# Optimization experiments

Measured on AMD Instinct MI355X. Metric: run time of the kernel, lower is better.

## Reference

```python
import jax, jax.numpy as jnp
import numpy as np

N, M, E = 14541, 237, 120000
XS, GS, HID, OUT, H = 100, 100, 100, 100, 2
NEG_SLOPE = 0.2


def _l2(v, axis):
    # F.normalize(p=2): x / clamp_min(||x||, 1e-12)
    return v / jnp.maximum(jnp.linalg.norm(v, axis=axis, keepdims=True), 1e-12)


def _rel_att(h_ijk, ends, n, W, b, w_att, out):
    # edge MLP -> [E, H, out]
    c = (h_ijk @ W.T + b).reshape(-1, H, out)
    # attention logits per edge/head, b_ijk = -leaky_relu(a_ijk)
    a = jnp.sum(w_att * c, axis=2, keepdims=True)            # [E, H, 1]
    e = jnp.exp(-jax.nn.leaky_relu(a, NEG_SLOPE))            # [E, H, 1]
    denom = jax.ops.segment_sum(e, ends, num_segments=n)     # [n, H, 1]
    alpha = e / denom[ends]                                  # scatter-softmax
    # self zero-edges in original == segment_sum zero-init; elu(0)=0 matches
    h = jax.ops.segment_sum(alpha * c, ends, num_segments=n) # [n, H, out]
    return jax.nn.elu(h)


def setup_inputs() -> dict:
    key = jax.random.key(0)
    ks = jax.random.split(key, 24)
    f32 = jnp.float32
    def w(k, shp, s=0.1):
        return jax.random.normal(k, shp, dtype=f32) * s
    inp = {
        "x": jax.random.normal(ks[0], (N, XS), dtype=f32),
        "g": jax.random.normal(ks[1], (M, GS), dtype=f32),
        # layer-1 inbound/outbound attention (fc1: [H*HID, 2*XS+GS])
        "W1in": w(ks[2], (H * HID, 2 * XS + GS)), "b1in": jnp.zeros((H * HID,), f32), "a1in": w(ks[3], (1, H, HID)),
        "W1out": w(ks[4], (H * HID, 2 * XS + GS)), "b1out": jnp.zeros((H * HID,), f32), "a1out": w(ks[5], (1, H, HID)),
        "Wa1": w(ks[6], (1, 2 * HID)), "ba1": jnp.zeros((1,), f32),
        # layer-2 attention (fc1: [H*OUT, 2*H*HID+GS])
        "W2in": w(ks[7], (H * OUT, 2 * H * HID + GS)), "b2in": jnp.zeros((H * OUT,), f32), "a2in": w(ks[8], (1, H, OUT)),
        "W2out": w(ks[9], (H * OUT, 2 * H * HID + GS)), "b2out": jnp.zeros((H * OUT,), f32), "a2out": w(ks[10], (1, H, OUT)),
        "Wa2": w(ks[11], (1, 2 * OUT)), "ba2": jnp.zeros((1,), f32),
        # entity residual projection and relation projection
        "Went": w(ks[12], (H * OUT, XS)), "bent": jnp.zeros((H * OUT,), f32),
        "Wrel": w(ks[13], (H * OUT, GS)), "brel": jnp.zeros((H * OUT,), f32),
        "edge_idx": jax.random.randint(ks[14], (2, E), 0, N),
        "edge_type": jax.random.randint(ks[15], (E,), 0, M),
    }
    return inp


def reference(x, g, W1in, b1in, a1in, W1out, b1out, a1out, Wa1, ba1,
              W2in, b2in, a2in, W2out, b2out, a2out, Wa2, ba2,
              Went, bent, Wrel, brel, edge_idx, edge_type):
    n = x.shape[0]
    xn = _l2(x, 1)
    row, col = edge_idx[0], edge_idx[1]
    # layer 1
    h_ijk = jnp.concatenate([xn[row], xn[col], g[edge_type]], axis=1)  # [E, 2*XS+GS]
    hin = _rel_att(h_ijk, col, n, W1in, b1in, a1in, HID)
    hout = _rel_att(h_ijk, row, n, W1out, b1out, a1out, HID)
    al = jax.nn.sigmoid(jnp.concatenate([hin, hout], axis=2) @ Wa1.T + ba1)  # [n, H, 1]
    h = al * hin + (1.0 - al) * hout
    h = _l2(jax.nn.elu(h), 2).reshape(n, H * HID)  # head-concat
    # layer 2
    h_ijk = jnp.concatenate([h[row], h[col], g[edge_type]], axis=1)  # [E, 2*H*HID+GS]
    hin = _rel_att(h_ijk, col, n, W2in, b2in, a2in, OUT)
    hout = _rel_att(h_ijk, row, n, W2out, b2out, a2out, OUT)
    al = jax.nn.sigmoid(jnp.concatenate([hin, hout], axis=2) @ Wa2.T + ba2)
    h = al * hin + (1.0 - al) * hout
    h = _l2(jax.nn.elu(h), 2)                       # [n, H, OUT]
    # entity residual + relation projection
    h_prime = (xn @ Went.T + bent).reshape(n, H, OUT) + h
    h_prime = _l2(h_prime, 2).reshape(n, H * OUT)
    g_prime = g @ Wrel.T + brel                     # [M, H*OUT]
    return h_prime, g_prime
```

## Files before the change

### kernel.cpp

```cpp
#include <hip/hip_runtime.h>
#include <math.h>

#define NSLOPE 0.2f

typedef unsigned short ushort_t;
typedef unsigned char uchar_t;
typedef __attribute__((ext_vector_type(8))) short bf16x8;
typedef __attribute__((ext_vector_type(8))) unsigned short ushort8;
typedef __attribute__((ext_vector_type(4))) float f32x4;

__device__ __forceinline__ float elu1(float x) { return x > 0.f ? x : expm1f(x); }

__device__ __forceinline__ ushort_t f2bf(float f) {
  union { float f; unsigned int u; } v; v.f = f;
  unsigned int r = v.u + 0x7fffu + ((v.u >> 16) & 1u);
  return (ushort_t)(r >> 16);
}
__device__ __forceinline__ float bf2f(ushort_t u) {
  union { unsigned int i; float f; } v; v.i = ((unsigned int)u) << 16; return v.f;
}
__device__ __forceinline__ uchar_t f2fp8(float f) {
  int pk = __builtin_amdgcn_cvt_pk_fp8_f32(f, f, 0, false);
  return (uchar_t)(pk & 0xff);
}


__device__ void dev_build_w(int idx,
                            const float* __restrict__ W1in, const float* __restrict__ W1out,
                            const float* __restrict__ W2in, const float* __restrict__ W2out,
                            const float* __restrict__ Went,
                            ushort_t* __restrict__ wcat1, ushort_t* __restrict__ wcat2,
                            ushort_t* __restrict__ wentb) {
  const int S1 = 832 * 128, S2 = 832 * 256, S3 = 256 * 128;
  if (idx < S1) {
    int ro = idx >> 7, k = idx & 127;
    float val = 0.f;
    if (ro < 800 && k < 100) {
      int o = ro / 200, cc = ro - o * 200;
      const float* W = (o < 2) ? W1in : W1out;
      val = W[(size_t)cc * 300 + (o & 1) * 100 + k];
    }
    wcat1[idx] = f2bf(val);
  } else if (idx < S1 + S2) {
    int i2 = idx - S1;
    int ro = i2 >> 8, k = i2 & 255;
    float val = 0.f;
    if (ro < 800 && k < 200) {
      int o = ro / 200, cc = ro - o * 200;
      const float* W = (o < 2) ? W2in : W2out;
      val = W[(size_t)cc * 500 + (o & 1) * 200 + k];
    }
    wcat2[i2] = f2bf(val);
  } else if (idx < S1 + S2 + S3) {
    int i3 = idx - S1 - S2;
    int ro = i3 >> 7, k = i3 & 127;
    float val = (ro < 200 && k < 100) ? Went[ro * 100 + k] : 0.f;
    wentb[i3] = f2bf(val);
  }
}

__device__ void dev_makeu(int idx,
                          const float* __restrict__ W1in, const float* __restrict__ a1in,
                          const float* __restrict__ W1out, const float* __restrict__ a1out,
                          const float* __restrict__ W2in, const float* __restrict__ a2in,
                          const float* __restrict__ W2out, const float* __restrict__ a2out,
                          float* __restrict__ u1in, float* __restrict__ u1out,
                          float* __restrict__ u2in, float* __restrict__ u2out) {
  if (idx >= 3200) return;
  const float* W; const float* avec; float* u; int Kp, local;
  if (idx < 600)       { W = W1in;  avec = a1in;  u = u1in;  Kp = 300; local = idx; }
  else if (idx < 1200) { W = W1out; avec = a1out; u = u1out; Kp = 300; local = idx - 600; }
  else if (idx < 2200) { W = W2in;  avec = a2in;  u = u2in;  Kp = 500; local = idx - 1200; }
  else                 { W = W2out; avec = a2out; u = u2out; Kp = 500; local = idx - 2200; }
  int h = local / Kp, kp = local - h * Kp;
  const float* Wb = W + (size_t)(h * 100) * Kp + kp;
  const float* ab = avec + h * 100;
  float s = 0.f;
  for (int k = 0; k < 100; ++k) s += ab[k] * Wb[(size_t)k * Kp];
  u[local] = s;
}

__device__ void dev_l2norm_q(int bb, int tid, const float* __restrict__ x,
                             ushort_t* __restrict__ xnb,
                             const float* __restrict__ u1in, const float* __restrict__ u1out,
                             float* __restrict__ qA, float* __restrict__ qB,
                             float* __restrict__ qC, float* __restrict__ qD, int N) {
  int wid = bb * 4 + (tid >> 6);
  int lane = tid & 63;
  if (wid >= N) return;
  const float* p = x + (size_t)wid * 100;
  float v0 = p[lane];
  bool t2 = lane < 36;
  float v1 = t2 ? p[lane + 64] : 0.f;
  float ss = v0 * v0 + v1 * v1;
#pragma unroll
  for (int m = 1; m < 64; m <<= 1) ss += __shfl_xor(ss, m, 64);
  float inv = 1.f / fmaxf(sqrtf(ss), 1e-12f);
  float a0 = v0 * inv, a1 = v1 * inv;
  ushort_t* ob = xnb + (size_t)wid * 128;
  ob[lane] = f2bf(a0);
  ob[64 + lane] = t2 ? f2bf(a1) : (ushort_t)0;
  int k0 = lane, k1 = 64 + lane;
  float s[8];
  s[0] = a0 * u1in[k0]        + (t2 ? a1 * u1in[k1]        : 0.f);
  s[1] = a0 * u1in[300 + k0]  + (t2 ? a1 * u1in[300 + k1]  : 0.f);
  s[2] = a0 * u1in[100 + k0]  + (t2 ? a1 * u1in[100 + k1]  : 0.f);
  s[3] = a0 * u1in[400 + k0]  + (t2 ? a1 * u1in[400 + k1]  : 0.f);
  s[4] = a0 * u1out[k0]       + (t2 ? a1 * u1out[k1]       : 0.f);
  s[5] = a0 * u1out[300 + k0] + (t2 ? a1 * u1out[300 + k1] : 0.f);
  s[6] = a0 * u1out[100 + k0] + (t2 ? a1 * u1out[100 + k1] : 0.f);
  s[7] = a0 * u1out[400 + k0] + (t2 ? a1 * u1out[400 + k1] : 0.f);
#pragma unroll
  for (int m = 1; m < 64; m <<= 1) {
#pragma unroll
    for (int i = 0; i < 8; ++i) s[i] += __shfl_xor(s[i], m, 64);
  }
  if (lane == 0) {
    qA[wid * 2] = s[0]; qA[wid * 2 + 1] = s[1];
    qB[wid * 2] = s[2]; qB[wid * 2 + 1] = s[3];
    qC[wid * 2] = s[4]; qC[wid * 2 + 1] = s[5];
    qD[wid * 2] = s[6]; qD[wid * 2 + 1] = s[7];
  }
}

__device__ void dev_qrel2(int bb, int tid, const float* __restrict__ g,
                          const float* __restrict__ u1in, const float* __restrict__ u1out,
                          const float* __restrict__ u2in, const float* __restrict__ u2out,
                          float* __restrict__ q3i1, float* __restrict__ q3o1,
                          float* __restrict__ q3i2, float* __restrict__ q3o2, int Mn) {
  int wid = bb * 4 + (tid >> 6);
  int lane = tid & 63;
  if (wid >= 2 * Mn) return;
  int lay = wid >= Mn;
  int m = wid - lay * Mn;
  const float* uin  = lay ? u2in  : u1in;
  const float* uout = lay ? u2out : u1out;
  int Kp = lay ? 500 : 300;
  int off3 = lay ? 400 : 200;
  float* q3i = lay ? q3i2 : q3i1;
  float* q3o = lay ? q3o2 : q3o1;
  const float* a = g + (size_t)m * 100;
  float s[4] = {0.f, 0.f, 0.f, 0.f};
  for (int k = lane; k < 100; k += 64) {
    float av = a[k];
    s[0] += av * uin[off3 + k];
    s[1] += av * uin[Kp + off3 + k];
    s[2] += av * uout[off3 + k];
    s[3] += av * uout[Kp + off3 + k];
  }
#pragma unroll
  for (int mm = 1; mm < 64; mm <<= 1) {
#pragma unroll
    for (int i = 0; i < 4; ++i) s[i] += __shfl_xor(s[i], mm, 64);
  }
  if (lane == 0) {
    q3i[m * 2] = s[0]; q3i[m * 2 + 1] = s[1];
    q3o[m * 2] = s[2]; q3o[m * 2 + 1] = s[3];
  }
}

__device__ void dev_count(int bb, int tid, const int* __restrict__ row,
                          const int* __restrict__ col,
                          int* __restrict__ cntIn, int* __restrict__ cntOut, int E) {
  int e = bb * 256 + tid;
  if (e >= E) return;
  atomicAdd(&cntIn[col[e]], 1);
  atomicAdd(&cntOut[row[e]], 1);
}

__device__ void dev_edge_e(int bb, int tid,
                           const int* __restrict__ row, const int* __restrict__ col,
                           const int* __restrict__ ety,
                           const float* __restrict__ qA, const float* __restrict__ qB,
                           const float* __restrict__ q3i,
                           const float* __restrict__ qC, const float* __restrict__ qD,
                           const float* __restrict__ q3o,
                           const int* __restrict__ invIn, const int* __restrict__ invOut,
                           float4* __restrict__ recI, float4* __restrict__ recO, int E) {
  int e = bb * 256 + tid;
  if (e >= E) return;
  int r = row[e], c = col[e], t = ety[e];
  float2 vA = *(const float2*)(qA + (size_t)r * 2);
  float2 vB = *(const float2*)(qB + (size_t)c * 2);
  float2 v3 = *(const float2*)(q3i + (size_t)t * 2);
  float2 vC = *(const float2*)(qC + (size_t)r * 2);
  float2 vD = *(const float2*)(qD + (size_t)c * 2);
  float2 v4 = *(const float2*)(q3o + (size_t)t * 2);
  float a0 = vA.x + vB.x + v3.x, a1 = vA.y + vB.y + v3.y;
  float b0 = vC.x + vD.x + v4.x, b1 = vC.y + vD.y + v4.y;
  float2 rI, rO;
  rI.x = expf(-(a0 > 0.f ? a0 : NSLOPE * a0));
  rI.y = expf(-(a1 > 0.f ? a1 : NSLOPE * a1));
  rO.x = expf(-(b0 > 0.f ? b0 : NSLOPE * b0));
  rO.y = expf(-(b1 > 0.f ? b1 : NSLOPE * b1));
  *(float2*)(recI + invIn[e]) = rI;
  *(float2*)(recO + invOut[e]) = rO;
}

__device__ void dev_mfma(int bx, int by, int tid,
                         ushort_t* __restrict__ smA, ushort_t* __restrict__ smB,
                         const ushort_t* __restrict__ Ab, int lda,
                         const ushort_t* __restrict__ Bb, int Kpad,
                         int R, int NC, int OUTW, const float* __restrict__ bias,
                         float* __restrict__ C0,
                         ushort_t* __restrict__ Bd0, ushort_t* __restrict__ Bd1,
                         ushort_t* __restrict__ Bd2, ushort_t* __restrict__ Bd3,
                         uchar_t* __restrict__ Q0, uchar_t* __restrict__ Q3) {
  const int lane = tid & 63;
  const int w = tid >> 6;
  const int wm = w >> 1, wn = w & 1;
  const int m0 = by * 64;
  const int n0 = bx * 64;
  const int srow = tid >> 2;
  const int sq = tid & 3;
  const int sw3 = srow & 7;
  const int sbase = srow * 64;
  const int so0 = sbase + ((((sq << 1) + 0) ^ sw3) << 3);
  const int so1 = sbase + ((((sq << 1) + 1) ^ sw3) << 3);
  const bool aok = (m0 + srow) < R;
  const ushort_t* Ag = Ab + (size_t)(m0 + srow) * lda + sq * 16;
  const ushort_t* Bg = Bb + (size_t)(n0 + srow) * Kpad + sq * 16;
  const int lswz = lane & 7;
  const int hi = lane >> 4;
  const int rA0 = (wm * 32 + (lane & 15)) * 64;
  const int rB0 = (wn * 32 + (lane & 15)) * 64;
  f32x4 acc[2][2] = {};
  for (int k0 = 0; k0 < Kpad; k0 += 64) {
    ushort8 a0 = {0, 0, 0, 0, 0, 0, 0, 0}, a1 = {0, 0, 0, 0, 0, 0, 0, 0};
    if (aok) {
      a0 = *(const ushort8*)(Ag + k0);
      a1 = *(const ushort8*)(Ag + k0 + 8);
    }
    ushort8 b0 = *(const ushort8*)(Bg + k0);
    ushort8 b1 = *(const ushort8*)(Bg + k0 + 8);
    __syncthreads();
    *(ushort8*)(smA + so0) = a0;
    *(ushort8*)(smA + so1) = a1;
    *(ushort8*)(smB + so0) = b0;
    *(ushort8*)(smB + so1) = b1;
    __syncthreads();
#pragma unroll
    for (int ks = 0; ks < 2; ++ks) {
      int co = (((ks << 2) + hi) ^ lswz) << 3;
      bf16x8 aA = *(const bf16x8*)(smA + rA0 + co);
      bf16x8 aB = *(const bf16x8*)(smA + rA0 + 1024 + co);
      bf16x8 bA = *(const bf16x8*)(smB + rB0 + co);
      bf16x8 bB = *(const bf16x8*)(smB + rB0 + 1024 + co);
      acc[0][0] = __builtin_amdgcn_mfma_f32_16x16x32_bf16(aA, bA, acc[0][0], 0, 0, 0);
      acc[0][1] = __builtin_amdgcn_mfma_f32_16x16x32_bf16(aA, bB, acc[0][1], 0, 0, 0);
      acc[1][0] = __builtin_amdgcn_mfma_f32_16x16x32_bf16(aB, bA, acc[1][0], 0, 0, 0);
      acc[1][1] = __builtin_amdgcn_mfma_f32_16x16x32_bf16(aB, bB, acc[1][1], 0, 0, 0);
    }
  }
  ushort_t* Bds[4] = {Bd0, Bd1, Bd2, Bd3};
#pragma unroll
  for (int mt = 0; mt < 2; ++mt) {
    int rr0 = m0 + wm * 32 + mt * 16 + (lane >> 4) * 4;
#pragma unroll
    for (int nt = 0; nt < 2; ++nt) {
      int cc = n0 + wn * 32 + nt * 16 + (lane & 15);
      if (cc < NC) {
        int o = cc / OUTW;
        int c2 = cc - o * OUTW;
        float bv = bias ? bias[c2] : 0.f;
        uchar_t* Q = (o == 0) ? Q0 : ((o == 3) ? Q3 : nullptr);
        ushort_t* Bd = Bds[o];
        if (Q) {
#pragma unroll
          for (int reg = 0; reg < 4; ++reg) {
            int r = rr0 + reg;
            if (r < R) Q[(size_t)r * OUTW + c2] = f2fp8(acc[mt][nt][reg] + bv);
          }
        } else if (Bd) {
#pragma unroll
          for (int reg = 0; reg < 4; ++reg) {
            int r = rr0 + reg;
            if (r < R) Bd[(size_t)r * OUTW + c2] = f2bf(acc[mt][nt][reg] + bv);
          }
        } else {
#pragma unroll
          for (int reg = 0; reg < 4; ++reg) {
            int r = rr0 + reg;
            if (r < R) C0[(size_t)r * OUTW + c2] = acc[mt][nt][reg] + bv;
          }
        }
      }
    }
  }
}

template <int NOUT, int BF>
__device__ void dev_gemm_multi(int bx, int by, int tid, float4 (*As)[25],
                               const float* __restrict__ A, int lda,
                               const float* __restrict__ W0, const float* __restrict__ W1,
                               int ldw,
                               const float* __restrict__ b0, const float* __restrict__ b1,
                               void* __restrict__ C0v, void* __restrict__ C1v, int R) {
  const int K4 = 25;
  int row0 = by * 32;
  {
    int r = tid >> 3;
    int rr = row0 + r;
    const float4* Ar = (const float4*)(A + (size_t)rr * lda);
    for (int k4 = (tid & 7); k4 < K4; k4 += 8)
      As[r][k4] = (rr < R) ? Ar[k4] : make_float4(0.f, 0.f, 0.f, 0.f);
  }
  __syncthreads();
  int c = bx * 64 + (tid & 63);
  if (c < 200) {
    int rb = (tid >> 6) << 3;
    const float4* Wr[NOUT];
    Wr[0] = (const float4*)(W0 + (size_t)c * ldw);
    if (NOUT > 1) Wr[1] = (const float4*)(W1 + (size_t)c * ldw);
    float acc[NOUT][8];
#pragma unroll
    for (int o = 0; o < NOUT; ++o)
#pragma unroll
      for (int i = 0; i < 8; ++i) acc[o][i] = 0.f;
#pragma unroll 2
    for (int k4 = 0; k4 < K4; ++k4) {
      float4 a[8];
#pragma unroll
      for (int i = 0; i < 8; ++i) a[i] = As[rb + i][k4];
#pragma unroll
      for (int o = 0; o < NOUT; ++o) {
        float4 wv = Wr[o][k4];
#pragma unroll
        for (int i = 0; i < 8; ++i)
          acc[o][i] += a[i].x * wv.x + a[i].y * wv.y + a[i].z * wv.z + a[i].w * wv.w;
      }
    }
    float bv[NOUT];
    bv[0] = b0 ? b0[c] : 0.f;
    if (NOUT > 1) bv[1] = b1 ? b1[c] : 0.f;
    void* Cp[NOUT];
    Cp[0] = C0v;
    if (NOUT > 1) Cp[1] = C1v;
#pragma unroll
    for (int i = 0; i < 8; ++i) {
      int rr = row0 + rb + i;
      if (rr < R) {
#pragma unroll
        for (int o = 0; o < NOUT; ++o) {
          float val = acc[o][i] + bv[o];
          if (BF) ((ushort_t*)Cp[o])[(size_t)rr * 200 + c] = f2bf(val);
          else    ((float*)Cp[o])[(size_t)rr * 200 + c] = val;
        }
      }
    }
  }
}


__global__ __launch_bounds__(256) void MEGA0(
    const float* W1in, const float* W1out, const float* W2in, const float* W2out,
    const float* Went,
    ushort_t* wcat1, ushort_t* wcat2, ushort_t* wentb,
    const float* a1in, const float* a1out, const float* a2in, const float* a2out,
    float* u1in, float* u1out, float* u2in, float* u2out,
    int* cntIn, int* cntOut, int N, int nb_bw, int nb_mk) {
  int b = blockIdx.x, tid = threadIdx.x;
  if (b < nb_bw) {
    dev_build_w(b * 256 + tid, W1in, W1out, W2in, W2out, Went, wcat1, wcat2, wentb);
  } else if (b < nb_bw + nb_mk) {
    dev_makeu((b - nb_bw) * 256 + tid, W1in, a1in, W1out, a1out, W2in, a2in, W2out, a2out,
              u1in, u1out, u2in, u2out);
  } else {
    int idx = (b - nb_bw - nb_mk) * 256 + tid;
    if (idx < N) cntIn[idx] = 0;
    else if (idx < 2 * N) cntOut[idx - N] = 0;
  }
}

__global__ __launch_bounds__(256) void MEGA1(
    const float* x, ushort_t* xnb, const float* u1in, const float* u1out,
    float* qA, float* qB, float* qC, float* qD, int N,
    const float* g, const float* u2in, const float* u2out,
    float* q3i1, float* q3o1, float* q3i2, float* q3o2, int Mn,
    const int* row, const int* col, int* cntIn, int* cntOut, int E,
    int nb_l2, int nb_qr) {
  int b = blockIdx.x, tid = threadIdx.x;
  if (b < nb_l2) {
    dev_l2norm_q(b, tid, x, xnb, u1in, u1out, qA, qB, qC, qD, N);
  } else if (b < nb_l2 + nb_qr) {
    dev_qrel2(b - nb_l2, tid, g, u1in, u1out, u2in, u2out, q3i1, q3o1, q3i2, q3o2, Mn);
  } else {
    dev_count(b - nb_l2 - nb_qr, tid, row, col, cntIn, cntOut, E);
  }
}

__global__ __launch_bounds__(256) void k_scanA(const int* __restrict__ cntIn,
                                               const int* __restrict__ cntOut,
                                               int* __restrict__ part, int N, int nbc) {
  __shared__ int wsum[4];
  int b = blockIdx.x;
  const int* cnt = (b < nbc) ? cntIn : cntOut;
  int cb = (b < nbc) ? b : b - nbc;
  int idx = cb * 256 + threadIdx.x;
  int v = (idx < N) ? cnt[idx] : 0;
#pragma unroll
  for (int m = 1; m < 64; m <<= 1) v += __shfl_xor(v, m, 64);
  if ((threadIdx.x & 63) == 0) wsum[threadIdx.x >> 6] = v;
  __syncthreads();
  if (threadIdx.x == 0) part[b] = wsum[0] + wsum[1] + wsum[2] + wsum[3];
}

__global__ __launch_bounds__(256) void k_scanB(int* __restrict__ part,
                                               int* __restrict__ rsIn, int* __restrict__ rsOut,
                                               int nbc, int N) {
  __shared__ int buf[512];
  int t = threadIdx.x;
  buf[t]       = (t < nbc) ? part[t] : 0;
  buf[256 + t] = (t < nbc) ? part[nbc + t] : 0;
  __syncthreads();
  for (int off = 1; off < 256; off <<= 1) {
    int v0 = (t >= off) ? buf[t - off] : 0;
    int v1 = (t >= off) ? buf[256 + t - off] : 0;
    __syncthreads();
    buf[t] += v0; buf[256 + t] += v1;
    __syncthreads();
  }
  if (t < nbc) {
    part[t]       = (t == 0) ? 0 : buf[t - 1];
    part[nbc + t] = (t == 0) ? 0 : buf[256 + t - 1];
  }
  if (t == 0) { rsIn[N] = buf[nbc - 1]; rsOut[N] = buf[256 + nbc - 1]; }
}

__global__ __launch_bounds__(256) void k_scanC(const int* __restrict__ cntIn,
                                               const int* __restrict__ cntOut,
                                               const int* __restrict__ part,
                                               int* __restrict__ rsIn, int* __restrict__ rsOut,
                                               int* __restrict__ posIn, int* __restrict__ posOut,
                                               int N, int nbc) {
  __shared__ int buf[256];
  int b = blockIdx.x;
  const int* cnt = (b < nbc) ? cntIn : cntOut;
  int* rs  = (b < nbc) ? rsIn : rsOut;
  int* pos = (b < nbc) ? posIn : posOut;
  int cb = (b < nbc) ? b : b - nbc;
  int base = part[b];
  int t = threadIdx.x;
  int idx = cb * 256 + t;
  buf[t] = (idx < N) ? cnt[idx] : 0;
  __syncthreads();
  for (int off = 1; off < 256; off <<= 1) {
    int v = (t >= off) ? buf[t - off] : 0;
    __syncthreads();
    buf[t] += v;
    __syncthreads();
  }
  if (idx < N) {
    int excl = base + ((t == 0) ? 0 : buf[t - 1]);
    rs[idx] = excl; pos[idx] = excl;
  }
}

__global__ void k_fill(const int* __restrict__ row, const int* __restrict__ col,
                       const int* __restrict__ ety,
                       int* __restrict__ posIn, int* __restrict__ posOut,
                       float4* __restrict__ recI, float4* __restrict__ recO,
                       int* __restrict__ invIn, int* __restrict__ invOut, int E) {
  int e = blockIdx.x * blockDim.x + threadIdx.x;
  if (e >= E) return;
  int r = row[e], c = col[e], tt = ety[e];
  int p = atomicAdd(&posIn[c], 1);
  ((int2*)(recI + p))[1] = make_int2(r, tt);
  invIn[e] = p;
  int q = atomicAdd(&posOut[r], 1);
  ((int2*)(recO + q))[1] = make_int2(c, tt);
  invOut[e] = q;
}

__global__ __launch_bounds__(256) void MEGA2(
    const ushort_t* xnb, const ushort_t* wcat1,
    uchar_t* PA8, ushort_t* PBb, ushort_t* PCb, uchar_t* PD8, int N,
    const int* row, const int* col, const int* ety,
    const float* qA, const float* qB, const float* q3i1,
    const float* qC, const float* qD, const float* q3o1,
    const int* invIn, const int* invOut, float4* recI, float4* recO, int E,
    const float* g, const float* W1in200, const float* W1out200,
    const float* b1in, const float* b1out, ushort_t* P3ib, ushort_t* P3ob,
    const float* W2in400, const float* W2out400,
    const float* b2in, const float* b2out, ushort_t* P3ib2, ushort_t* P3ob2, int Mn,
    const ushort_t* wentb, const float* bent, ushort_t* hentb,
    const float* Wrel, const float* brel, float* outg,
    int nb_mf, int nb_ee, int nb_gm, int nb_we) {
  __shared__ float4 shbuf4[1024];
  ushort_t* smA = (ushort_t*)shbuf4;
  ushort_t* smB = smA + 64 * 64;
  float4 (*As)[25] = (float4(*)[25])shbuf4;
  int b = blockIdx.x, tid = threadIdx.x;
  if (b < nb_mf) {
    dev_mfma(b % 13, b / 13, tid, smA, smB, xnb, 128, wcat1, 128, N, 800, 200, nullptr,
             nullptr, nullptr, PBb, PCb, nullptr, PA8, PD8);
  } else if ((b -= nb_mf) < nb_ee) {
    dev_edge_e(b, tid, row, col, ety, qA, qB, q3i1, qC, qD, q3o1,
               invIn, invOut, recI, recO, E);
  } else if ((b -= nb_ee) < nb_gm) {
    dev_gemm_multi<2, 1>(b & 3, b >> 2, tid, As, g, 100, W1in200, W1out200, 300,
                         b1in, b1out, P3ib, P3ob, Mn);
  } else if ((b -= nb_gm) < nb_gm) {
    dev_gemm_multi<2, 1>(b & 3, b >> 2, tid, As, g, 100, W2in400, W2out400, 500,
                         b2in, b2out, P3ib2, P3ob2, Mn);
  } else if ((b -= nb_gm) < nb_we) {
    dev_mfma(b & 3, b >> 2, tid, smA, smB, xnb, 128, wentb, 128, N, 200, 200, bent,
             nullptr, hentb, nullptr, nullptr, nullptr, nullptr, nullptr);
  } else {
    b -= nb_we;
    dev_gemm_multi<1, 0>(b & 3, b >> 2, tid, As, g, 100, Wrel, nullptr, 100,
                         brel, nullptr, outg, nullptr, Mn);
  }
}

__global__ __launch_bounds__(256) void MEGA3(
    const ushort_t* h1b, const ushort_t* wcat2,
    uchar_t* PA8, ushort_t* PBb, ushort_t* PCb, uchar_t* PD8, int N,
    const int* row, const int* col, const int* ety,
    const float* qA, const float* qB, const float* q3i2,
    const float* qC, const float* qD, const float* q3o2,
    const int* invIn, const int* invOut, float4* recI, float4* recO, int E,
    int nb_mf) {
  __shared__ float4 shbuf4[1024];
  ushort_t* smA = (ushort_t*)shbuf4;
  ushort_t* smB = smA + 64 * 64;
  int b = blockIdx.x, tid = threadIdx.x;
  if (b < nb_mf) {
    dev_mfma(b % 13, b / 13, tid, smA, smB, h1b, 256, wcat2, 256, N, 800, 200, nullptr,
             nullptr, nullptr, PBb, PCb, nullptr, PA8, PD8);
  } else {
    dev_edge_e(b - nb_mf, tid, row, col, ety, qA, qB, q3i2, qC, qD, q3o2,
               invIn, invOut, recI, recO, E);
  }
}

__global__ void k_node_att(const float4* __restrict__ recI, const int* __restrict__ rsIn,
                           const float4* __restrict__ recO, const int* __restrict__ rsOut,
                           const uchar_t* __restrict__ PA8, const ushort_t* __restrict__ PBb,
                           const ushort_t* __restrict__ PCb, const uchar_t* __restrict__ PD8,
                           const ushort_t* __restrict__ P3ib, const ushort_t* __restrict__ P3ob,
                           const float* __restrict__ Wg, const float* __restrict__ bg,
                           const float* __restrict__ u2in, const float* __restrict__ u2out,
                           float* __restrict__ qA, float* __restrict__ qB,
                           float* __restrict__ qC, float* __restrict__ qD,
                           ushort_t* __restrict__ Hb,
                           const ushort_t* __restrict__ hentb, float* __restrict__ outp, int N) {
  __shared__ float4 sRecI[4][64];
  __shared__ float4 sRecO[4][64];
  int wv = threadIdx.x >> 6;
  int wid  = (int)((blockIdx.x * (unsigned)blockDim.x + threadIdx.x) >> 6);
  int lane = threadIdx.x & 63;
  if (wid >= N) return;
  int n = wid;
  int half = lane >> 5, i = lane & 31;
  bool act = i < 25;
  int j = half * 100 + i * 4;
  int sIn = rsIn[n], degIn = rsIn[n + 1] - sIn;
  int sOut = rsOut[n], degOut = rsOut[n + 1] - sOut;
  float4 accIn = {0.f, 0.f, 0.f, 0.f}, accOut = {0.f, 0.f, 0.f, 0.f};
  float dI0 = 0.f, dI1 = 0.f, dO0 = 0.f, dO1 = 0.f;
  int mx = max(degIn, degOut);
  for (int b = 0; b < mx; b += 64) {
    int l = b + lane;
    if (l < degIn) {
      float4 rc = recI[sIn + l];
      dI0 += rc.x; dI1 += rc.y;
      sRecI[wv][lane] = rc;
    }
    if (l < degOut) {
      float4 rc = recO[sOut + l];
      dO0 += rc.x; dO1 += rc.y;
      sRecO[wv][lane] = rc;
    }
    int mI = degIn - b;  if (mI > 64) mI = 64;
    int mO = degOut - b; if (mO > 64) mO = 64;
    int m2 = max(mI, mO);
    for (int jj = 0; jj < m2; ++jj) {
      if (act && jj < mI) {
        float4 rc = sRecI[wv][jj];
        int rI = __float_as_int(rc.z), tI = __float_as_int(rc.w);
        float wgt = half ? rc.y : rc.x;
        int paw = *(const int*)(PA8 + (size_t)rI * 200 + j);
        ushort4 p3 = *(const ushort4*)(P3ib + (size_t)tI * 200 + j);
        accIn.x += wgt * (__builtin_amdgcn_cvt_f32_fp8(paw, 0) + bf2f(p3.x));
        accIn.y += wgt * (__builtin_amdgcn_cvt_f32_fp8(paw, 1) + bf2f(p3.y));
        accIn.z += wgt * (__builtin_amdgcn_cvt_f32_fp8(paw, 2) + bf2f(p3.z));
        accIn.w += wgt * (__builtin_amdgcn_cvt_f32_fp8(paw, 3) + bf2f(p3.w));
      }
      if (act && jj < mO) {
        float4 rc = sRecO[wv][jj];
        int rO = __float_as_int(rc.z), tO = __float_as_int(rc.w);
        float wgt = half ? rc.y : rc.x;
        int pdw = *(const int*)(PD8 + (size_t)rO * 200 + j);
        ushort4 p3 = *(const ushort4*)(P3ob + (size_t)tO * 200 + j);
        accOut.x += wgt * (__builtin_amdgcn_cvt_f32_fp8(pdw, 0) + bf2f(p3.x));
        accOut.y += wgt * (__builtin_amdgcn_cvt_f32_fp8(pdw, 1) + bf2f(p3.y));
        accOut.z += wgt * (__builtin_amdgcn_cvt_f32_fp8(pdw, 2) + bf2f(p3.z));
        accOut.w += wgt * (__builtin_amdgcn_cvt_f32_fp8(pdw, 3) + bf2f(p3.w));
      }
    }
  }
#pragma unroll
  for (int m = 1; m < 64; m <<= 1) {
    dI0 += __shfl_xor(dI0, m, 64); dI1 += __shfl_xor(dI1, m, 64);
    dO0 += __shfl_xor(dO0, m, 64); dO1 += __shfl_xor(dO1, m, 64);
  }
  float4 hin = {0.f, 0.f, 0.f, 0.f}, hout = {0.f, 0.f, 0.f, 0.f};
  if (degIn > 0 && act) {
    float invd = 1.f / (half ? dI1 : dI0);
    ushort4 ps = *(const ushort4*)(PBb + (size_t)n * 200 + j);
    hin.x = elu1(bf2f(ps.x) + accIn.x * invd);
    hin.y = elu1(bf2f(ps.y) + accIn.y * invd);
    hin.z = elu1(bf2f(ps.z) + accIn.z * invd);
    hin.w = elu1(bf2f(ps.w) + accIn.w * invd);
  }
  if (degOut > 0 && act) {
    float invd = 1.f / (half ? dO1 : dO0);
    ushort4 ps = *(const ushort4*)(PCb + (size_t)n * 200 + j);
    hout.x = elu1(bf2f(ps.x) + accOut.x * invd);
    hout.y = elu1(bf2f(ps.y) + accOut.y * invd);
    hout.z = elu1(bf2f(ps.z) + accOut.z * invd);
    hout.w = elu1(bf2f(ps.w) + accOut.w * invd);
  }
  float gp = 0.f;
  if (act) {
    int k = i * 4;
    gp = Wg[k] * hin.x + Wg[k + 1] * hin.y + Wg[k + 2] * hin.z + Wg[k + 3] * hin.w +
         Wg[100 + k] * hout.x + Wg[100 + k + 1] * hout.y +
         Wg[100 + k + 2] * hout.z + Wg[100 + k + 3] * hout.w;
  }
#pragma unroll
  for (int m = 1; m < 32; m <<= 1) gp += __shfl_xor(gp, m, 32);
  float al = 1.f / (1.f + expf(-(gp + bg[0])));
  float4 he;
  he.x = elu1(al * hin.x + (1.f - al) * hout.x);
  he.y = elu1(al * hin.y + (1.f - al) * hout.y);
  he.z = elu1(al * hin.z + (1.f - al) * hout.z);
  he.w = elu1(al * hin.w + (1.f - al) * hout.w);
  float ss = he.x * he.x + he.y * he.y + he.z * he.z + he.w * he.w;
#pragma unroll
  for (int m = 1; m < 32; m <<= 1) ss += __shfl_xor(ss, m, 32);
  float inv = 1.f / fmaxf(sqrtf(ss), 1e-12f);
  float4 o = {he.x * inv, he.y * inv, he.z * inv, he.w * inv};
  if (Hb) {
    if (act) {
      ushort4 ov; ov.x = f2bf(o.x); ov.y = f2bf(o.y); ov.z = f2bf(o.z); ov.w = f2bf(o.w);
      *(ushort4*)(Hb + (size_t)n * 256 + j) = ov;
    } else {
      int pi = half * 7 + (i - 25);
      ushort4 z = {0, 0, 0, 0};
      *(ushort4*)(Hb + (size_t)n * 256 + 200 + pi * 4) = z;
    }
  }
  if (outp) {
    float4 v = {0.f, 0.f, 0.f, 0.f};
    if (act) {
      ushort4 hv = *(const ushort4*)(hentb + (size_t)n * 200 + j);
      v.x = bf2f(hv.x) + o.x; v.y = bf2f(hv.y) + o.y;
      v.z = bf2f(hv.z) + o.z; v.w = bf2f(hv.w) + o.w;
    }
    float s2 = v.x * v.x + v.y * v.y + v.z * v.z + v.w * v.w;
#pragma unroll
    for (int m = 1; m < 32; m <<= 1) s2 += __shfl_xor(s2, m, 32);
    float inv2 = 1.f / fmaxf(sqrtf(s2), 1e-12f);
    if (act) {
      float4 ov = {v.x * inv2, v.y * inv2, v.z * inv2, v.w * inv2};
      *(float4*)(outp + (size_t)n * 200 + j) = ov;
    }
  }
  if (u2in) {
    float4 ov = act ? o : make_float4(0.f, 0.f, 0.f, 0.f);
    float s[8];
#pragma unroll
    for (int h = 0; h < 2; ++h) {
      float4 uA = *(const float4*)(u2in + h * 500 + j);
      float4 uB = *(const float4*)(u2in + h * 500 + 200 + j);
      float4 uC = *(const float4*)(u2out + h * 500 + j);
      float4 uD = *(const float4*)(u2out + h * 500 + 200 + j);
      s[0 + h] = ov.x * uA.x + ov.y * uA.y + ov.z * uA.z + ov.w * uA.w;
      s[2 + h] = ov.x * uB.x + ov.y * uB.y + ov.z * uB.z + ov.w * uB.w;
      s[4 + h] = ov.x * uC.x + ov.y * uC.y + ov.z * uC.z + ov.w * uC.w;
      s[6 + h] = ov.x * uD.x + ov.y * uD.y + ov.z * uD.z + ov.w * uD.w;
    }
#pragma unroll
    for (int m = 1; m < 64; m <<= 1) {
#pragma unroll
      for (int ii = 0; ii < 8; ++ii) s[ii] += __shfl_xor(s[ii], m, 64);
    }
    if (lane == 0) {
      qA[n * 2] = s[0]; qA[n * 2 + 1] = s[1];
      qB[n * 2] = s[2]; qB[n * 2 + 1] = s[3];
      qC[n * 2] = s[4]; qC[n * 2 + 1] = s[5];
      qD[n * 2] = s[6]; qD[n * 2 + 1] = s[7];
    }
  }
}

extern "C" void kernel_launch(void* const* d_in, const int* in_sizes, int n_in,
                              void* d_out, int out_size, void* d_ws, size_t ws_size,
                              hipStream_t stream) {
  const float* x    = (const float*)d_in[0];
  const float* g    = (const float*)d_in[1];
  const float* W1in = (const float*)d_in[2];
  const float* b1in = (const float*)d_in[3];
  const float* a1in = (const float*)d_in[4];
  const float* W1out= (const float*)d_in[5];
  const float* b1out= (const float*)d_in[6];
  const float* a1out= (const float*)d_in[7];
  const float* Wa1  = (const float*)d_in[8];
  const float* ba1  = (const float*)d_in[9];
  const float* W2in = (const float*)d_in[10];
  const float* b2in = (const float*)d_in[11];
  const float* a2in = (const float*)d_in[12];
  const float* W2out= (const float*)d_in[13];
  const float* b2out= (const float*)d_in[14];
  const float* a2out= (const float*)d_in[15];
  const float* Wa2  = (const float*)d_in[16];
  const float* ba2  = (const float*)d_in[17];
  const float* Went = (const float*)d_in[18];
  const float* bent = (const float*)d_in[19];
  const float* Wrel = (const float*)d_in[20];
  const float* brel = (const float*)d_in[21];
  const int*  eidx  = (const int*)d_in[22];
  const int*  ety   = (const int*)d_in[23];

  const int N = in_sizes[0] / 100;
  const int M = in_sizes[1] / 100;
  const int E = in_sizes[23];
  const int* row = eidx;
  const int* col = eidx + E;
  float* out = (float*)d_out;

  float* ws = (float*)d_ws;
  size_t off = 0;
  auto alloc = [&](size_t nf) { float* p = ws + off; off += (nf + 3) & ~(size_t)3; return p; };
  float4* recI = (float4*)alloc((size_t)E * 4);
  float4* recO = (float4*)alloc((size_t)E * 4);
  uchar_t* PA8 = (uchar_t*)alloc((size_t)N * 50);
  uchar_t* PD8 = (uchar_t*)alloc((size_t)N * 50);
  ushort_t* PBb = (ushort_t*)alloc((size_t)N * 100);
  ushort_t* PCb = (ushort_t*)alloc((size_t)N * 100);
  ushort_t* P3ib = (ushort_t*)alloc((size_t)M * 100);
  ushort_t* P3ob = (ushort_t*)alloc((size_t)M * 100);
  ushort_t* P3ib2 = (ushort_t*)alloc((size_t)M * 100);
  ushort_t* P3ob2 = (ushort_t*)alloc((size_t)M * 100);
  ushort_t* xnb = (ushort_t*)alloc((size_t)N * 64);
  ushort_t* h1b = (ushort_t*)alloc((size_t)N * 128);
  ushort_t* hentb = (ushort_t*)alloc((size_t)N * 100);
  ushort_t* wcat1 = (ushort_t*)alloc((size_t)832 * 64);
  ushort_t* wcat2 = (ushort_t*)alloc((size_t)832 * 128);
  ushort_t* wentb = (ushort_t*)alloc((size_t)256 * 64);
  float* qA  = alloc((size_t)N * 2);
  float* qB  = alloc((size_t)N * 2);
  float* qC  = alloc((size_t)N * 2);
  float* qD  = alloc((size_t)N * 2);
  float* q3i1 = alloc((size_t)M * 2);
  float* q3o1 = alloc((size_t)M * 2);
  float* q3i2 = alloc((size_t)M * 2);
  float* q3o2 = alloc((size_t)M * 2);
  int* invIn  = (int*)alloc((size_t)E);
  int* invOut = (int*)alloc((size_t)E);
  float* u1in  = alloc(600);
  float* u1out = alloc(600);
  float* u2in  = alloc(1000);
  float* u2out = alloc(1000);
  int* cntIn  = (int*)alloc((size_t)N);
  int* cntOut = (int*)alloc((size_t)N);
  int* rsIn   = (int*)alloc((size_t)N + 1);
  int* rsOut  = (int*)alloc((size_t)N + 1);
  int* posIn  = (int*)alloc((size_t)N);
  int* posOut = (int*)alloc((size_t)N);
  int* part   = (int*)alloc((size_t)512);

  const int gN4 = (N + 3) / 4;
  const int gE  = (E + 255) / 256;
  const int mT  = (N + 63) / 64;
  const int nbc = (N + 255) / 256;

  const int nb_bw = (832 * 128 + 832 * 256 + 256 * 128 + 255) / 256;
  const int nb_mk = 13;
  const int nb_z  = (2 * N + 255) / 256;
  const int nb_l2 = gN4;
  const int nb_qr = (2 * M + 3) / 4;
  const int nb_mf = 13 * mT;
  const int nb_gm = 4 * ((M + 31) / 32);
  const int nb_we = 4 * mT;

  MEGA0<<<nb_bw + nb_mk + nb_z, 256, 0, stream>>>(
      W1in, W1out, W2in, W2out, Went, wcat1, wcat2, wentb,
      a1in, a1out, a2in, a2out, u1in, u1out, u2in, u2out,
      cntIn, cntOut, N, nb_bw, nb_mk);

  MEGA1<<<nb_l2 + nb_qr + gE, 256, 0, stream>>>(
      x, xnb, u1in, u1out, qA, qB, qC, qD, N,
      g, u2in, u2out, q3i1, q3o1, q3i2, q3o2, M,
      row, col, cntIn, cntOut, E, nb_l2, nb_qr);

  k_scanA<<<2 * nbc, 256, 0, stream>>>(cntIn, cntOut, part, N, nbc);
  k_scanB<<<1, 256, 0, stream>>>(part, rsIn, rsOut, nbc, N);
  k_scanC<<<2 * nbc, 256, 0, stream>>>(cntIn, cntOut, part, rsIn, rsOut, posIn, posOut, N, nbc);
  k_fill<<<gE, 256, 0, stream>>>(row, col, ety, posIn, posOut, recI, recO, invIn, invOut, E);

  MEGA2<<<nb_mf + gE + nb_gm * 3 + nb_we, 256, 0, stream>>>(
      xnb, wcat1, PA8, PBb, PCb, PD8, N,
      row, col, ety, qA, qB, q3i1, qC, qD, q3o1, invIn, invOut, recI, recO, E,
      g, W1in + 200, W1out + 200, b1in, b1out, P3ib, P3ob,
      W2in + 400, W2out + 400, b2in, b2out, P3ib2, P3ob2, M,
      wentb, bent, hentb, Wrel, brel, out + (size_t)N * 200,
      nb_mf, gE, nb_gm, nb_we);

  k_node_att<<<gN4, 256, 0, stream>>>(recI, rsIn, recO, rsOut,
                                      PA8, PBb, PCb, PD8, P3ib, P3ob, Wa1, ba1,
                                      u2in, u2out, qA, qB, qC, qD,
                                      h1b, nullptr, nullptr, N);

  MEGA3<<<nb_mf + gE, 256, 0, stream>>>(
      h1b, wcat2, PA8, PBb, PCb, PD8, N,
      row, col, ety, qA, qB, q3i2, qC, qD, q3o2, invIn, invOut, recI, recO, E,
      nb_mf);

  k_node_att<<<gN4, 256, 0, stream>>>(recI, rsIn, recO, rsOut,
                                      PA8, PBb, PCb, PD8, P3ib2, P3ob2, Wa2, ba2,
                                      nullptr, nullptr, qA, qB, qC, qD,
                                      nullptr, hentb, out, N);
}
```

Measured before the change: 185.2 us.

## Fuse edge attention logit computation into node aggregation kernel

Result: no change. 182.3 us (median of 2 runs) (-1.6%).

```diff
diff --git a/kernel.cpp b/kernel.cpp
--- a/kernel.cpp
+++ b/kernel.cpp
@@ -166,35 +166,6 @@
   if (e >= E) return;
   atomicAdd(&cntIn[col[e]], 1);
   atomicAdd(&cntOut[row[e]], 1);
-}
-
-__device__ void dev_edge_e(int bb, int tid,
-                           const int* __restrict__ row, const int* __restrict__ col,
-                           const int* __restrict__ ety,
-                           const float* __restrict__ qA, const float* __restrict__ qB,
-                           const float* __restrict__ q3i,
-                           const float* __restrict__ qC, const float* __restrict__ qD,
-                           const float* __restrict__ q3o,
-                           const int* __restrict__ invIn, const int* __restrict__ invOut,
-                           float4* __restrict__ recI, float4* __restrict__ recO, int E) {
-  int e = bb * 256 + tid;
-  if (e >= E) return;
-  int r = row[e], c = col[e], t = ety[e];
-  float2 vA = *(const float2*)(qA + (size_t)r * 2);
-  float2 vB = *(const float2*)(qB + (size_t)c * 2);
-  float2 v3 = *(const float2*)(q3i + (size_t)t * 2);
-  float2 vC = *(const float2*)(qC + (size_t)r * 2);
-  float2 vD = *(const float2*)(qD + (size_t)c * 2);
-  float2 v4 = *(const float2*)(q3o + (size_t)t * 2);
-  float a0 = vA.x + vB.x + v3.x, a1 = vA.y + vB.y + v3.y;
-  float b0 = vC.x + vD.x + v4.x, b1 = vC.y + vD.y + v4.y;
-  float2 rI, rO;
-  rI.x = expf(-(a0 > 0.f ? a0 : NSLOPE * a0));
-  rI.y = expf(-(a1 > 0.f ? a1 : NSLOPE * a1));
-  rO.x = expf(-(b0 > 0.f ? b0 : NSLOPE * b0));
-  rO.y = expf(-(b1 > 0.f ? b1 : NSLOPE * b1));
-  *(float2*)(recI + invIn[e]) = rI;
-  *(float2*)(recO + invOut[e]) = rO;
 }
 
 __device__ void dev_mfma(int bx, int by, int tid,
@@ -459,33 +430,26 @@
 __global__ void k_fill(const int* __restrict__ row, const int* __restrict__ col,
                        const int* __restrict__ ety,
                        int* __restrict__ posIn, int* __restrict__ posOut,
-                       float4* __restrict__ recI, float4* __restrict__ recO,
-                       int* __restrict__ invIn, int* __restrict__ invOut, int E) {
+                       int2* __restrict__ pinIn, int2* __restrict__ pinOut, int E) {
   int e = blockIdx.x * blockDim.x + threadIdx.x;
   if (e >= E) return;
   int r = row[e], c = col[e], tt = ety[e];
   int p = atomicAdd(&posIn[c], 1);
-  ((int2*)(recI + p))[1] = make_int2(r, tt);
-  invIn[e] = p;
+  pinIn[p] = make_int2(r, tt);
   int q = atomicAdd(&posOut[r], 1);
-  ((int2*)(recO + q))[1] = make_int2(c, tt);
-  invOut[e] = q;
+  pinOut[q] = make_int2(c, tt);
 }
 
 __global__ __launch_bounds__(256) void MEGA2(
     const ushort_t* xnb, const ushort_t* wcat1,
     uchar_t* PA8, ushort_t* PBb, ushort_t* PCb, uchar_t* PD8, int N,
-    const int* row, const int* col, const int* ety,
-    const float* qA, const float* qB, const float* q3i1,
-    const float* qC, const float* qD, const float* q3o1,
-    const int* invIn, const int* invOut, float4* recI, float4* recO, int E,
     const float* g, const float* W1in200, const float* W1out200,
     const float* b1in, const float* b1out, ushort_t* P3ib, ushort_t* P3ob,
     const float* W2in400, const float* W2out400,
     const float* b2in, const float* b2out, ushort_t* P3ib2, ushort_t* P3ob2, int Mn,
     const ushort_t* wentb, const float* bent, ushort_t* hentb,
     const float* Wrel, const float* brel, float* outg,
-    int nb_mf, int nb_ee, int nb_gm, int nb_we) {
+    int nb_mf, int nb_gm, int nb_we) {
   __shared__ float4 shbuf4[1024];
   ushort_t* smA = (ushort_t*)shbuf4;
   ushort_t* smB = smA + 64 * 64;
@@ -494,10 +458,7 @@
   if (b < nb_mf) {
     dev_mfma(b % 13, b / 13, tid, smA, smB, xnb, 128, wcat1, 128, N, 800, 200, nullptr,
              nullptr, nullptr, PBb, PCb, nullptr, PA8, PD8);
-  } else if ((b -= nb_mf) < nb_ee) {
-    dev_edge_e(b, tid, row, col, ety, qA, qB, q3i1, qC, qD, q3o1,
-               invIn, invOut, recI, recO, E);
-  } else if ((b -= nb_ee) < nb_gm) {
+  } else if ((b -= nb_mf) < nb_gm) {
     dev_gemm_multi<2, 1>(b & 3, b >> 2, tid, As, g, 100, W1in200, W1out200, 300,
                          b1in, b1out, P3ib, P3ob, Mn);
   } else if ((b -= nb_gm) < nb_gm) {
@@ -515,34 +476,26 @@
 
 __global__ __launch_bounds__(256) void MEGA3(
     const ushort_t* h1b, const ushort_t* wcat2,
-    uchar_t* PA8, ushort_t* PBb, ushort_t* PCb, uchar_t* PD8, int N,
-    const int* row, const int* col, const int* ety,
-    const float* qA, const float* qB, const float* q3i2,
-    const float* qC, const float* qD, const float* q3o2,
-    const int* invIn, const int* invOut, float4* recI, float4* recO, int E,
-    int nb_mf) {
+    uchar_t* PA8, ushort_t* PBb, ushort_t* PCb, uchar_t* PD8, int N) {
   __shared__ float4 shbuf4[1024];
   ushort_t* smA = (ushort_t*)shbuf4;
   ushort_t* smB = smA + 64 * 64;
-  int b = blockIdx.x, tid = threadIdx.x;
-  if (b < nb_mf) {
-    dev_mfma(b % 13, b / 13, tid, smA, smB, h1b, 256, wcat2, 256, N, 800, 200, nullptr,
-             nullptr, nullptr, PBb, PCb, nullptr, PA8, PD8);
-  } else {
-    dev_edge_e(b - nb_mf, tid, row, col, ety, qA, qB, q3i2, qC, qD, q3o2,
-               invIn, invOut, recI, recO, E);
-  }
-}
-
-__global__ void k_node_att(const float4* __restrict__ recI, const int* __restrict__ rsIn,
-                           const float4* __restrict__ recO, const int* __restrict__ rsOut,
+  dev_mfma(blockIdx.x % 13, blockIdx.x / 13, threadIdx.x, smA, smB, h1b, 256, wcat2, 256,
+           N, 800, 200, nullptr, nullptr, nullptr, PBb, PCb, nullptr, PA8, PD8);
+}
+
+__global__ void k_node_att(const int2* __restrict__ pinIn, const int* __restrict__ rsIn,
+                           const int2* __restrict__ pinOut, const int* __restrict__ rsOut,
                            const uchar_t* __restrict__ PA8, const ushort_t* __restrict__ PBb,
                            const ushort_t* __restrict__ PCb, const uchar_t* __restrict__ PD8,
                            const ushort_t* __restrict__ P3ib, const ushort_t* __restrict__ P3ob,
+                           const float* __restrict__ qAin, const float* __restrict__ qBin,
+                           const float* __restrict__ qCin, const float* __restrict__ qDin,
+                           const float* __restrict__ q3i, const float* __restrict__ q3o,
                            const float* __restrict__ Wg, const float* __restrict__ bg,
                            const float* __restrict__ u2in, const float* __restrict__ u2out,
-                           float* __restrict__ qA, float* __restrict__ qB,
-                           float* __restrict__ qC, float* __restrict__ qD,
+                           float* __restrict__ qAo, float* __restrict__ qBo,
+                           float* __restrict__ qCo, float* __restrict__ qDo,
                            ushort_t* __restrict__ Hb,
                            const ushort_t* __restrict__ hentb, float* __restrict__ outp, int N) {
   __shared__ float4 sRecI[4][64];
@@ -557,19 +510,33 @@
   int j = half * 100 + i * 4;
   int sIn = rsIn[n], degIn = rsIn[n + 1] - sIn;
   int sOut = rsOut[n], degOut = rsOut[n + 1] - sOut;
+  float2 qBn = *(const float2*)(qBin + (size_t)n * 2);
+  float2 qCn = *(const float2*)(qCin + (size_t)n * 2);
   float4 accIn = {0.f, 0.f, 0.f, 0.f}, accOut = {0.f, 0.f, 0.f, 0.f};
   float dI0 = 0.f, dI1 = 0.f, dO0 = 0.f, dO1 = 0.f;
   int mx = max(degIn, degOut);
   for (int b = 0; b < mx; b += 64) {
     int l = b + lane;
     if (l < degIn) {
-      float4 rc = recI[sIn + l];
-      dI0 += rc.x; dI1 += rc.y;
+      int2 pt = pinIn[sIn + l];
+      float2 qp = *(const float2*)(qAin + (size_t)pt.x * 2);
+      float2 q3 = *(const float2*)(q3i + (size_t)pt.y * 2);
+      float a0 = qp.x + qBn.x + q3.x, a1 = qp.y + qBn.y + q3.y;
+      float e0 = expf(-(a0 > 0.f ? a0 : NSLOPE * a0));
+      float e1 = expf(-(a1 > 0.f ? a1 : NSLOPE * a1));
+      dI0 += e0; dI1 += e1;
+      float4 rc = {e0, e1, __int_as_float(pt.x), __int_as_float(pt.y)};
       sRecI[wv][lane] = rc;
     }
     if (l < degOut) {
-      float4 rc = recO[sOut + l];
-      dO0 += rc.x; dO1 += rc.y;
+      int2 pt = pinOut[sOut + l];
+      float2 qp = *(const float2*)(qDin + (size_t)pt.x * 2);
+      float2 q3 = *(const float2*)(q3o + (size_t)pt.y * 2);
+      float b0 = qCn.x + qp.x + q3.x, b1 = qCn.y + qp.y + q3.y;
+      float e0 = expf(-(b0 > 0.f ? b0 : NSLOPE * b0));
+      float e1 = expf(-(b1 > 0.f ? b1 : NSLOPE * b1));
+      dO0 += e0; dO1 += e1;
+      float4 rc = {e0, e1, __int_as_float(pt.x), __int_as_float(pt.y)};
       sRecO[wv][lane] = rc;
     }
     int mI = degIn - b;  if (mI > 64) mI = 64;
@@ -688,10 +655,10 @@
       for (int ii = 0; ii < 8; ++ii) s[ii] += __shfl_xor(s[ii], m, 64);
     }
     if (lane == 0) {
-      qA[n * 2] = s[0]; qA[n * 2 + 1] = s[1];
-      qB[n * 2] = s[2]; qB[n * 2 + 1] = s[3];
-      qC[n * 2] = s[4]; qC[n * 2 + 1] = s[5];
-      qD[n * 2] = s[6]; qD[n * 2 + 1] = s[7];
+      qAo[n * 2] = s[0]; qAo[n * 2 + 1] = s[1];
+      qBo[n * 2] = s[2]; qBo[n * 2 + 1] = s[3];
+      qCo[n * 2] = s[4]; qCo[n * 2 + 1] = s[5];
+      qDo[n * 2] = s[6]; qDo[n * 2 + 1] = s[7];
     }
   }
 }
@@ -734,8 +701,8 @@
   float* ws = (float*)d_ws;
   size_t off = 0;
   auto alloc = [&](size_t nf) { float* p = ws + off; off += (nf + 3) & ~(size_t)3; return p; };
-  float4* recI = (float4*)alloc((size_t)E * 4);
-  float4* recO = (float4*)alloc((size_t)E * 4);
+  int2* pinIn  = (int2*)alloc((size_t)E * 2);
+  int2* pinOut = (int2*)alloc((size_t)E * 2);
   uchar_t* PA8 = (uchar_t*)alloc((size_t)N * 50);
   uchar_t* PD8 = (uchar_t*)alloc((size_t)N * 50);
   ushort_t* PBb = (ushort_t*)alloc((size_t)N * 100);
@@ -754,12 +721,14 @@
   float* qB  = alloc((size_t)N * 2);
   float* qC  = alloc((size_t)N * 2);
   float* qD  = alloc((size_t)N * 2);
+  float* qA2 = alloc((size_t)N * 2);
+  float* qB2 = alloc((size_t)N * 2);
+  float* qC2 = alloc((size_t)N * 2);
+  float* qD2 = alloc((size_t)N * 2);
   float* q3i1 = alloc((size_t)M * 2);
   float* q3o1 = alloc((size_t)M * 2);
   float* q3i2 = alloc((size_t)M * 2);
   float* q3o2 = alloc((size_t)M * 2);
-  int* invIn  = (int*)alloc((size_t)E);
-  int* invOut = (int*)alloc((size_t)E);
   float* u1in  = alloc(600);
   float* u1out = alloc(600);
   float* u2in  = alloc(1000);
@@ -799,28 +768,26 @@
   k_scanA<<<2 * nbc, 256, 0, stream>>>(cntIn, cntOut, part, N, nbc);
   k_scanB<<<1, 256, 0, stream>>>(part, rsIn, rsOut, nbc, N);
   k_scanC<<<2 * nbc, 256, 0, stream>>>(cntIn, cntOut, part, rsIn, rsOut, posIn, posOut, N, nbc);
-  k_fill<<<gE, 256, 0, stream>>>(row, col, ety, posIn, posOut, recI, recO, invIn, invOut, E);
-
-  MEGA2<<<nb_mf + gE + nb_gm * 3 + nb_we, 256, 0, stream>>>(
+  k_fill<<<gE, 256, 0, stream>>>(row, col, ety, posIn, posOut, pinIn, pinOut, E);
+
+  MEGA2<<<nb_mf + nb_gm * 3 + nb_we, 256, 0, stream>>>(
       xnb, wcat1, PA8, PBb, PCb, PD8, N,
-      row, col, ety, qA, qB, q3i1, qC, qD, q3o1, invIn, invOut, recI, recO, E,
       g, W1in + 200, W1out + 200, b1in, b1out, P3ib, P3ob,
       W2in + 400, W2out + 400, b2in, b2out, P3ib2, P3ob2, M,
       wentb, bent, hentb, Wrel, brel, out + (size_t)N * 200,
-      nb_mf, gE, nb_gm, nb_we);
-
-  k_node_att<<<gN4, 256, 0, stream>>>(recI, rsIn, recO, rsOut,
-                                      PA8, PBb, PCb, PD8, P3ib, P3ob, Wa1, ba1,
-                                      u2in, u2out, qA, qB, qC, qD,
+      nb_mf, nb_gm, nb_we);
+
+  k_node_att<<<gN4, 256, 0, stream>>>(pinIn, rsIn, pinOut, rsOut,
+                                      PA8, PBb, PCb, PD8, P3ib, P3ob,
+                                      qA, qB, qC, qD, q3i1, q3o1, Wa1, ba1,
+                                      u2in, u2out, qA2, qB2, qC2, qD2,
                                       h1b, nullptr, nullptr, N);
 
-  MEGA3<<<nb_mf + gE, 256, 0, stream>>>(
-      h1b, wcat2, PA8, PBb, PCb, PD8, N,
-      row, col, ety, qA, qB, q3i2, qC, qD, q3o2, invIn, invOut, recI, recO, E,
-      nb_mf);
-
-  k_node_att<<<gN4, 256, 0, stream>>>(recI, rsIn, recO, rsOut,
-                                      PA8, PBb, PCb, PD8, P3ib2, P3ob2, Wa2, ba2,
-                                      nullptr, nullptr, qA, qB, qC, qD,
+  MEGA3<<<nb_mf, 256, 0, stream>>>(h1b, wcat2, PA8, PBb, PCb, PD8, N);
+
+  k_node_att<<<gN4, 256, 0, stream>>>(pinIn, rsIn, pinOut, rsOut,
+                                      PA8, PBb, PCb, PD8, P3ib2, P3ob2,
+                                      qA2, qB2, qC2, qD2, q3i2, q3o2, Wa2, ba2,
+                                      nullptr, nullptr, nullptr, nullptr, nullptr, nullptr,
                                       nullptr, hentb, out, N);
 }
```
